# Performance work log

Hardware: AMD Instinct MI355X
Metric: run time of the kernel (lower is better)

## Reference

```python
import jax, jax.numpy as jnp
import numpy as np

N_ATOMS = 100          # n_atoms from init_kwargs
BATCH = 1024           # dataset / batch size (single-batch usage per docstring)


def setup_inputs() -> dict:
    key = jax.random.key(0)
    k1, k2 = jax.random.split(key)
    # descriptors = pairwise distances between atoms -> 6 nonzero derivs per desc per frame
    ii, jj = np.triu_indices(N_ATOMS, 1)               # [D] each
    D = ii.shape[0]                                    # 4950 descriptors
    atoms = np.stack([ii, jj], axis=1)                 # [D, 2]
    atom_pd = np.repeat(atoms, 3, axis=1).reshape(-1)  # [D*6]: i,i,i,j,j,j per desc
    dim_pd = np.tile(np.array([0, 1, 2, 0, 1, 2]), D)  # [D*6]
    des_pd = np.repeat(np.arange(D), 6)                # [D*6]

    batch_ind = np.repeat(np.arange(BATCH), D * 6)     # [nnz]
    des_ind = np.tile(des_pd, BATCH)                   # [nnz]
    atom_ind = np.tile(atom_pd, BATCH)                 # [nnz]
    dim_ind = np.tile(dim_pd, BATCH)                   # [nnz]
    # faithful shifted index: per-frame offset + atom*3 + dim
    scatter_idx = batch_ind * (N_ATOMS * 3) + atom_ind * 3 + dim_ind

    nnz = batch_ind.shape[0]
    x = jax.random.normal(k1, (BATCH, D), dtype=jnp.float32)      # dq/d(descriptors)
    left = jax.random.normal(k2, (nnz,), dtype=jnp.float32)       # nonzero d(desc)/d(pos)
    return {
        "x": x,
        "left": left,
        "batch_ind": jnp.asarray(batch_ind, jnp.int32),
        "des_ind": jnp.asarray(des_ind, jnp.int32),
        "scatter_idx": jnp.asarray(scatter_idx, jnp.int32),
    }


def reference(x, left, batch_ind, des_ind, scatter_idx):
    # gather right operand: dq/d(desc) for each nonzero left entry
    right = x[batch_ind, des_ind]                      # [nnz]
    src = left * right                                 # chain rule terms
    # scatter-add into (frame, atom, dim) bins, then square (square modulus comps)
    acc = jax.ops.segment_sum(src, scatter_idx, num_segments=BATCH * N_ATOMS * 3)
    return (acc * acc).reshape(BATCH, N_ATOMS * 3)
```

## Files before the change

kernel.cpp:

```cpp
#include <hip/hip_runtime.h>
#include <math.h>


#define N_ATOMS 100
#define D_DESC  4950
#define BATCH   1024
#define NOUT    (N_ATOMS * 3)

__device__ __forceinline__ int rowstart(int i) {
    return (i * (2 * N_ATOMS - 1 - i)) >> 1;
}

__global__ __launch_bounds__(256, 4)
void SmartDerivatives_kernel(const float* __restrict__ x,
                             const float* __restrict__ left,
                             float* __restrict__ out) {
    __shared__ float acc[NOUT];
    const int b   = blockIdx.x;
    const int tid = threadIdx.x;

    for (int t = tid; t < NOUT; t += 256) acc[t] = 0.0f;
    __syncthreads();

    const float* __restrict__ xb = x    + (size_t)b * D_DESC;
    const float* __restrict__ lb = left + (size_t)b * D_DESC * 6;

    for (int d = tid; d < D_DESC; d += 256) {
        const float xv = xb[d];
        const float fr = 39601.0f - 8.0f * (float)d;
        int i = (int)((199.0f - sqrtf(fr)) * 0.5f);
        while (rowstart(i + 1) <= d) ++i;
        while (rowstart(i) > d) --i;
        const int j = d - rowstart(i) + i + 1;

        const float* lp = lb + (size_t)d * 6;
        const float l3 = lp[3], l4 = lp[4], l5 = lp[5];
        atomicAdd(&acc[j * 3 + 0], l3 * xv);
        atomicAdd(&acc[j * 3 + 1], l4 * xv);
        atomicAdd(&acc[j * 3 + 2], l5 * xv);
    }

    const int wave = tid >> 6;
    const int lane = tid & 63;
    for (int a = wave; a < N_ATOMS - 1; a += 4) {
        const int rs  = rowstart(a);
        const int len = N_ATOMS - 1 - a;
        float s0 = 0.0f, s1 = 0.0f, s2 = 0.0f;
        for (int l = lane; l < len; l += 64) {
            const int d = rs + l;
            const float xv = xb[d];
            const float* lp = lb + (size_t)d * 6;
            s0 += lp[0] * xv;
            s1 += lp[1] * xv;
            s2 += lp[2] * xv;
        }
        #pragma unroll
        for (int off = 32; off > 0; off >>= 1) {
            s0 += __shfl_down(s0, off, 64);
            s1 += __shfl_down(s1, off, 64);
            s2 += __shfl_down(s2, off, 64);
        }
        if (lane == 0) {
            atomicAdd(&acc[a * 3 + 0], s0);
            atomicAdd(&acc[a * 3 + 1], s1);
            atomicAdd(&acc[a * 3 + 2], s2);
        }
    }

    __syncthreads();

    float* __restrict__ ob = out + (size_t)b * NOUT;
    for (int t = tid; t < NOUT; t += 256) {
        const float v = acc[t];
        ob[t] = v * v;
    }
}

extern "C" void kernel_launch(void* const* d_in, const int* in_sizes, int n_in,
                              void* d_out, int out_size, void* d_ws, size_t ws_size,
                              hipStream_t stream) {
    const float* x    = (const float*)d_in[0];
    const float* left = (const float*)d_in[1];
    float* out = (float*)d_out;
    SmartDerivatives_kernel<<<BATCH, 256, 0, stream>>>(x, left, out);
}
```

Before: 387.4 us.

## Map lanes to atom pairs, drop shared atomics, use DPP wave reductions

Restructures the per-frame work so each wave processes rows i of the pair triangle, with each lane owning a partner atom j. The j-side contributions then build up in registers per lane instead of going through shared-memory atomics, and the i-side sums use a DPP-based wave reduction. Per-wave partials are combined in shared memory at the end. Each lane also loads all six left entries as float2 vectors, the sqrt-based index inversion is removed, and the block grows to 512 threads. The cost is extra masked lanes on short rows and more shared memory for the per-wave partials.

```diff
diff --git a/kernel.cpp b/kernel.cpp
--- a/kernel.cpp
+++ b/kernel.cpp
@@ -1,77 +1,103 @@
 #include <hip/hip_runtime.h>
-#include <math.h>
 
 
 #define N_ATOMS 100
 #define D_DESC  4950
 #define BATCH   1024
-#define NOUT    (N_ATOMS * 3)
+#define NOUT    300
+#define NWAVES  8
 
-__device__ __forceinline__ int rowstart(int i) {
-    return (i * (2 * N_ATOMS - 1 - i)) >> 1;
+template<int CTRL, int RMASK>
+__device__ __forceinline__ float dpp_step(float v) {
+    int s = __builtin_amdgcn_update_dpp(0, __float_as_int(v), CTRL, RMASK, 0xf, true);
+    return v + __int_as_float(s);
+}
+__device__ __forceinline__ float wave_sum(float v) {
+    v = dpp_step<0x111, 0xf>(v);
+    v = dpp_step<0x112, 0xf>(v);
+    v = dpp_step<0x114, 0xf>(v);
+    v = dpp_step<0x118, 0xf>(v);
+    v = dpp_step<0x142, 0xa>(v);
+    v = dpp_step<0x143, 0xc>(v);
+    return v;
 }
 
-__global__ __launch_bounds__(256, 4)
-void SmartDerivatives_kernel(const float* __restrict__ x,
-                             const float* __restrict__ left,
-                             float* __restrict__ out) {
-    __shared__ float acc[NOUT];
-    const int b   = blockIdx.x;
-    const int tid = threadIdx.x;
+__global__ __launch_bounds__(512, 4)
+void sd_kernel(const float* __restrict__ x,
+               const float* __restrict__ left,
+               float* __restrict__ out) {
+    __shared__ float rowacc[NOUT];
+    __shared__ float part[NWAVES][NOUT];
+    const int b    = blockIdx.x;
+    const int tid  = threadIdx.x;
+    const int w    = tid >> 6;
+    const int lane = tid & 63;
 
-    for (int t = tid; t < NOUT; t += 256) acc[t] = 0.0f;
+    for (int t = tid; t < NOUT; t += 512) rowacc[t] = 0.0f;
     __syncthreads();
 
     const float* __restrict__ xb = x    + (size_t)b * D_DESC;
     const float* __restrict__ lb = left + (size_t)b * D_DESC * 6;
 
-    for (int d = tid; d < D_DESC; d += 256) {
-        const float xv = xb[d];
-        const float fr = 39601.0f - 8.0f * (float)d;
-        int i = (int)((199.0f - sqrtf(fr)) * 0.5f);
-        while (rowstart(i + 1) <= d) ++i;
-        while (rowstart(i) > d) --i;
-        const int j = d - rowstart(i) + i + 1;
+    float a0 = 0.f, a1 = 0.f, a2 = 0.f;
+    float b0 = 0.f, b1 = 0.f, b2 = 0.f;
 
-        const float* lp = lb + (size_t)d * 6;
-        const float l3 = lp[3], l4 = lp[4], l5 = lp[5];
-        atomicAdd(&acc[j * 3 + 0], l3 * xv);
-        atomicAdd(&acc[j * 3 + 1], l4 * xv);
-        atomicAdd(&acc[j * 3 + 2], l5 * xv);
-    }
+    for (int i = w; i < N_ATOMS - 1; i += NWAVES) {
+        const int base = (i * (2 * N_ATOMS - 1 - i)) >> 1;
+        float s0 = 0.f, s1 = 0.f, s2 = 0.f;
 
-    const int wave = tid >> 6;
-    const int lane = tid & 63;
-    for (int a = wave; a < N_ATOMS - 1; a += 4) {
-        const int rs  = rowstart(a);
-        const int len = N_ATOMS - 1 - a;
-        float s0 = 0.0f, s1 = 0.0f, s2 = 0.0f;
-        for (int l = lane; l < len; l += 64) {
-            const int d = rs + l;
-            const float xv = xb[d];
-            const float* lp = lb + (size_t)d * 6;
-            s0 += lp[0] * xv;
-            s1 += lp[1] * xv;
-            s2 += lp[2] * xv;
+        if (i < 63) {
+            const int  j = lane;
+            const bool v = j > i;
+            const int  d = base + (v ? (j - i - 1) : 0);
+            const float2* lp = (const float2*)(lb + (size_t)d * 6);
+            const float2 c01 = lp[0];
+            const float2 c23 = lp[1];
+            const float2 c45 = lp[2];
+            const float  xv  = xb[d];
+            const float  m   = v ? xv : 0.f;
+            s0 += c01.x * m;  s1 += c01.y * m;  s2 += c23.x * m;
+            a0 += c23.y * m;  a1 += c45.x * m;  a2 += c45.y * m;
         }
-        #pragma unroll
-        for (int off = 32; off > 0; off >>= 1) {
-            s0 += __shfl_down(s0, off, 64);
-            s1 += __shfl_down(s1, off, 64);
-            s2 += __shfl_down(s2, off, 64);
+        {
+            const int  j = 64 + lane;
+            const bool v = (j < N_ATOMS) && (j > i);
+            const int  d = base + (v ? (j - i - 1) : 0);
+            const float2* lp = (const float2*)(lb + (size_t)d * 6);
+            const float2 c01 = lp[0];
+            const float2 c23 = lp[1];
+            const float2 c45 = lp[2];
+            const float  xv  = xb[d];
+            const float  m   = v ? xv : 0.f;
+            s0 += c01.x * m;  s1 += c01.y * m;  s2 += c23.x * m;
+            b0 += c23.y * m;  b1 += c45.x * m;  b2 += c45.y * m;
         }
-        if (lane == 0) {
-            atomicAdd(&acc[a * 3 + 0], s0);
-            atomicAdd(&acc[a * 3 + 1], s1);
-            atomicAdd(&acc[a * 3 + 2], s2);
+
+        s0 = wave_sum(s0);
+        s1 = wave_sum(s1);
+        s2 = wave_sum(s2);
+        if (lane == 63) {
+            rowacc[i * 3 + 0] = s0;
+            rowacc[i * 3 + 1] = s1;
+            rowacc[i * 3 + 2] = s2;
         }
     }
 
+    part[w][lane * 3 + 0] = a0;
+    part[w][lane * 3 + 1] = a1;
+    part[w][lane * 3 + 2] = a2;
+    if (lane < N_ATOMS - 64) {
+        part[w][(64 + lane) * 3 + 0] = b0;
+        part[w][(64 + lane) * 3 + 1] = b1;
+        part[w][(64 + lane) * 3 + 2] = b2;
+    }
     __syncthreads();
 
     float* __restrict__ ob = out + (size_t)b * NOUT;
-    for (int t = tid; t < NOUT; t += 256) {
-        const float v = acc[t];
+    for (int t = tid; t < NOUT; t += 512) {
+        float v = rowacc[t];
+        #pragma unroll
+        for (int q = 0; q < NWAVES; ++q) v += part[q][t];
         ob[t] = v * v;
     }
 }
@@ -82,5 +108,5 @@
     const float* x    = (const float*)d_in[0];
     const float* left = (const float*)d_in[1];
     float* out = (float*)d_out;
-    SmartDerivatives_kernel<<<BATCH, 256, 0, stream>>>(x, left, out);
+    sd_kernel<<<BATCH, 512, 0, stream>>>(x, left, out);
 }
```

Result: faster. 337.1 us (-13.0%).
